# Performance work log

Measured on AMD Instinct MI355X. Metric: run time of the kernel, lower is better.

The kernel has to match this reference:

```python
import jax, jax.numpy as jnp
import numpy as np

E = 768   # embed_size
H = 64    # head_embed_size
B = 8
T = 4096  # == ctx_size


def setup_inputs() -> dict:
    key = jax.random.key(0)
    k1, k2, k3, k4 = jax.random.split(key, 4)
    inputs = jax.random.normal(k1, (B, T, E), dtype=jnp.float32)
    # Linear weights stored as (E, H) so projection is x @ W
    scale = 1.0 / np.sqrt(E)
    Wq = jax.random.uniform(k2, (E, H), dtype=jnp.float32, minval=-scale, maxval=scale)
    Wk = jax.random.uniform(k3, (E, H), dtype=jnp.float32, minval=-scale, maxval=scale)
    Wv = jax.random.uniform(k4, (E, H), dtype=jnp.float32, minval=-scale, maxval=scale)
    return {"inputs": inputs, "Wq": Wq, "Wk": Wk, "Wv": Wv}


def reference(inputs, Wq, Wk, Wv):
    Tlen = inputs.shape[1]
    q = inputs @ Wq  # (B,T,H)
    k = inputs @ Wk  # (B,T,H)
    v = inputs @ Wv  # (B,T,H)
    # NOTE: original module does NOT scale by 1/sqrt(H) — faithful reproduction.
    scores = jnp.einsum('bqh,bkh->bqk', q, k)  # (B,T,T)
    causal = jnp.tril(jnp.ones((Tlen, Tlen), dtype=bool))
    scores = jnp.where(causal, scores, -jnp.inf)
    attn = jax.nn.softmax(scores, axis=-1)
    # dropout=0 -> identity
    out = jnp.einsum('bqk,bkh->bqh', attn, v)  # (B,T,H)
    return out
```

## Files before the change

### kernel.cpp

```cpp
#include <hip/hip_runtime.h>
#include <hip/hip_bf16.h>

#define E_DIM 768
#define H_DIM 64
#define B_SZ 8
#define T_SZ 4096
#define BT (B_SZ * T_SZ)

typedef __attribute__((ext_vector_type(8))) short short8;
typedef __attribute__((ext_vector_type(4))) float floatx4;

#define RAWBAR() __asm__ volatile("s_waitcnt lgkmcnt(0)\n\ts_barrier" ::: "memory")

static __device__ __forceinline__ unsigned short bf1(float a) {
    __hip_bfloat16 h = __float2bfloat16(a);
    unsigned short u; __builtin_memcpy(&u, &h, 2); return u;
}
static __device__ __forceinline__ unsigned int pk2(float a, float b) {
    __hip_bfloat162 h = __float22bfloat162_rn(float2{a, b});
    unsigned int u; __builtin_memcpy(&u, &h, 4); return u;
}

__global__ __launch_bounds__(256) void prep_w(
    const float* __restrict__ Wq, const float* __restrict__ Wk,
    const float* __restrict__ Wv, unsigned short* __restrict__ Wt)
{
    __shared__ float Ls[64][65];
    const int nt = blockIdx.x;
    const int kc = blockIdx.y;
    const float* __restrict__ W = (nt == 0) ? Wq : (nt == 1) ? Wk : Wv;
    const float scl = (nt == 0) ? 1.44269504088896f : 1.0f;
    const int t = threadIdx.x;
    const int k0 = kc * 64;

#pragma unroll
    for (int it = 0; it < 16; ++it) {
        const int kk = (t >> 6) + it * 4;
        Ls[kk][t & 63] = W[(size_t)(k0 + kk) * H_DIM + (t & 63)];
    }
    __syncthreads();

#pragma unroll
    for (int it = 0; it < 4; ++it) {
        const int nl = (t >> 4) + it * 16;
        const int kl = (t & 15) * 4;
        unsigned int u[2];
        u[0] = pk2(Ls[kl + 0][nl] * scl, Ls[kl + 1][nl] * scl);
        u[1] = pk2(Ls[kl + 2][nl] * scl, Ls[kl + 3][nl] * scl);
        *(uint2*)(Wt + (size_t)(nt * 64 + nl) * E_DIM + k0 + kl) = *(uint2*)u;
    }
}

__global__ __launch_bounds__(768) void proj_mfma(
    const float* __restrict__ X, const unsigned short* __restrict__ Wt,
    unsigned short* __restrict__ Qb, unsigned short* __restrict__ Kb,
    unsigned short* __restrict__ Vtb)
{
    __shared__ unsigned short Xs[2][16][776];

    const int tid  = threadIdx.x;
    const int wave = tid >> 6, lane = tid & 63;
    const int row  = lane & 15, quad = lane >> 4;
    const int m0   = blockIdx.x * 128;

    short8 bfr[24];
    {
        const unsigned short* wp = Wt + (size_t)(wave * 16 + row) * E_DIM + quad * 8;
#pragma unroll
        for (int ks = 0; ks < 24; ++ks) bfr[ks] = *(const short8*)(wp + ks * 32);
    }

    const int srow = tid & 15;
    const int sc   = tid >> 4;
    const float* __restrict__ xbase = X + (size_t)(m0 + srow) * E_DIM + sc * 16;

    float4 fx[4];
#define LDX(mt)                                                               \
    {                                                                         \
        const float* p = xbase + (size_t)(mt) * 16 * E_DIM;                   \
        fx[0] = *(const float4*)(p);     fx[1] = *(const float4*)(p + 4);     \
        fx[2] = *(const float4*)(p + 8); fx[3] = *(const float4*)(p + 12);    \
    }
#define STX(buf)                                                              \
    {                                                                         \
        unsigned int tmp[8];                                                  \
        tmp[0] = pk2(fx[0].x, fx[0].y); tmp[1] = pk2(fx[0].z, fx[0].w);       \
        tmp[2] = pk2(fx[1].x, fx[1].y); tmp[3] = pk2(fx[1].z, fx[1].w);       \
        tmp[4] = pk2(fx[2].x, fx[2].y); tmp[5] = pk2(fx[2].z, fx[2].w);       \
        tmp[6] = pk2(fx[3].x, fx[3].y); tmp[7] = pk2(fx[3].z, fx[3].w);       \
        *(int4*)&Xs[buf][srow][sc * 16]     = *(int4*)&tmp[0];                \
        *(int4*)&Xs[buf][srow][sc * 16 + 8] = *(int4*)&tmp[4];                \
    }

    LDX(0); STX(0); LDX(1);
    RAWBAR();

    const int g  = wave >> 2;
    const int h  = (wave & 3) * 16 + row;
    unsigned short* __restrict__ OQK = (g == 0) ? Qb : Kb;
    const int bb = m0 >> 12;

    int cur = 0;
    for (int mt = 0; mt < 8; ++mt) {
        if (mt < 7) STX(cur ^ 1);
        if (mt < 6) LDX(mt + 2);

        floatx4 a0 = (floatx4)0.0f, a1 = (floatx4)0.0f;
        floatx4 a2 = (floatx4)0.0f, a3 = (floatx4)0.0f;
#pragma unroll
        for (int ks = 0; ks < 6; ++ks) {
            const short8 f0 = *(const short8*)&Xs[cur][row][(ks * 4 + 0) * 32 + quad * 8];
            const short8 f1 = *(const short8*)&Xs[cur][row][(ks * 4 + 1) * 32 + quad * 8];
            const short8 f2 = *(const short8*)&Xs[cur][row][(ks * 4 + 2) * 32 + quad * 8];
            const short8 f3 = *(const short8*)&Xs[cur][row][(ks * 4 + 3) * 32 + quad * 8];
            a0 = __builtin_amdgcn_mfma_f32_16x16x32_bf16(f0, bfr[ks * 4 + 0], a0, 0, 0, 0);
            a1 = __builtin_amdgcn_mfma_f32_16x16x32_bf16(f1, bfr[ks * 4 + 1], a1, 0, 0, 0);
            a2 = __builtin_amdgcn_mfma_f32_16x16x32_bf16(f2, bfr[ks * 4 + 2], a2, 0, 0, 0);
            a3 = __builtin_amdgcn_mfma_f32_16x16x32_bf16(f3, bfr[ks * 4 + 3], a3, 0, 0, 0);
        }
        floatx4 acc;
#pragma unroll
        for (int r = 0; r < 4; ++r) acc[r] = (a0[r] + a1[r]) + (a2[r] + a3[r]);

        const int mr = m0 + mt * 16 + quad * 4;
        if (g < 2) {
#pragma unroll
            for (int r = 0; r < 4; ++r)
                OQK[(size_t)(mr + r) * H_DIM + h] = bf1(acc[r]);
        } else {
            const int t0 = mr & 4095;
            unsigned int u[2];
            u[0] = pk2(acc[0], acc[1]); u[1] = pk2(acc[2], acc[3]);
            *(uint2*)(Vtb + ((size_t)bb * H_DIM + h) * T_SZ + t0) = *(uint2*)u;
        }

        RAWBAR();
        cur ^= 1;
    }
#undef LDX
#undef STX
}

__global__ __launch_bounds__(256, 6) void attn_mfma(
    const unsigned short* __restrict__ Qb,
    const unsigned short* __restrict__ Kb,
    const unsigned short* __restrict__ Vtb,
    float* __restrict__ Opart, float* __restrict__ lpart,
    float* __restrict__ Out)
{
    __shared__ __align__(16) unsigned short KV[2][64][72];

    const int lb = blockIdx.x;
    const int b  = lb & 7;
    const int s  = lb >> 3;
    int qq, c, m;
    if (s < 24)       { m = 6; qq = 60 + s / 6;                        c = s % 6; }
    else if (s < 84)  { m = 5; const int i = s - 24;  qq = 48 + i / 5;    c = i % 5; }
    else if (s < 132) { m = 4; const int i = s - 84;  qq = 36 + (i >> 2); c = i & 3; }
    else if (s < 168) { m = 3; const int i = s - 132; qq = 24 + i / 3;    c = i % 3; }
    else if (s < 192) { m = 2; const int i = s - 168; qq = 12 + (i >> 1); c = i & 1; }
    else              { m = 1; qq = s - 192; c = 0; }
    const int ntot = qq + 1;
    const int k0t  = (c * ntot) / m;
    const int k1t  = ((c + 1) * ntot) / m;
    const int ktd  = ntot - 1;
    const int n    = k1t - k0t;
    const bool split = (m > 1);

    const int tid  = threadIdx.x;
    const int wq   = tid >> 6;
    const int lane = tid & 63;
    const int col  = lane & 15, quad = lane >> 4;

    const size_t base = (size_t)b * T_SZ * H_DIM;
    const int q0  = qq * 64;

    short8 qf0, qf1;
    {
        const unsigned short* qp = Qb + base + (size_t)(q0 + wq * 16 + col) * H_DIM + quad * 8;
        qf0 = *(const short8*)(qp);
        qf1 = *(const short8*)(qp + 32);
    }

    floatx4 o[4];
#pragma unroll
    for (int i = 0; i < 4; ++i) o[i] = (floatx4)0.0f;
    float lp = 0.0f;

    const int krow = tid >> 2, kcol = (tid & 3) * 16;
    const int kprow = (krow & 32) + ((krow >> 2) & 1) * 16 + ((krow & 31) >> 3) * 4 + (krow & 3);
    const unsigned short* __restrict__ Ksrc = Kb + base + (size_t)krow * H_DIM + kcol;
    const unsigned short* __restrict__ Vsrc = Vtb + ((size_t)b * H_DIM + krow) * T_SZ + kcol;

    int4 kr0, kr1, vr0, vr1;
#define LDKV(t)                                                          \
    {                                                                    \
        const unsigned short* kp = Ksrc + (size_t)(t) * 64 * H_DIM;      \
        kr0 = *(const int4*)kp; kr1 = *(const int4*)(kp + 8);            \
        const unsigned short* vp = Vsrc + (t) * 64;                      \
        vr0 = *(const int4*)vp; vr1 = *(const int4*)(vp + 8);            \
    }
#define STKV()                                                           \
    {                                                                    \
        *(int4*)&KV[0][kprow][kcol] = kr0; *(int4*)&KV[0][kprow][kcol + 8] = kr1; \
        *(int4*)&KV[1][krow][kcol] = vr0; *(int4*)&KV[1][krow][kcol + 8] = vr1; \
    }

    LDKV(k0t);
    STKV();
    if (n > 1) LDKV(k0t + 1);
    RAWBAR();

    for (int i = 0; i < n; ++i) {
        const int kt = k0t + i;

#pragma unroll
        for (int j = 0; j < 2; ++j) {
            floatx4 a0 = (floatx4)0.0f, a1 = (floatx4)0.0f;
            __builtin_amdgcn_s_setprio(1);
            {
                const unsigned short* kp0 = &KV[0][j * 32 + col][quad * 8];
                const unsigned short* kp1 = &KV[0][j * 32 + 16 + col][quad * 8];
                a0 = __builtin_amdgcn_mfma_f32_16x16x32_bf16(*(const short8*)(kp0),      qf0, a0, 0, 0, 0);
                a1 = __builtin_amdgcn_mfma_f32_16x16x32_bf16(*(const short8*)(kp1),      qf0, a1, 0, 0, 0);
                a0 = __builtin_amdgcn_mfma_f32_16x16x32_bf16(*(const short8*)(kp0 + 32), qf1, a0, 0, 0, 0);
                a1 = __builtin_amdgcn_mfma_f32_16x16x32_bf16(*(const short8*)(kp1 + 32), qf1, a1, 0, 0, 0);
            }
            __builtin_amdgcn_s_setprio(0);

            if (kt == ktd) {
                const int qg = q0 + wq * 16 + col;
                const int kb = kt * 64 + j * 32 + quad * 8;
#pragma unroll
                for (int r = 0; r < 4; ++r) {
                    if (kb + r > qg)     a0[r] = -1e30f;
                    if (kb + 4 + r > qg) a1[r] = -1e30f;
                }
            }

            const float p0 = exp2f(a0[0]), p1 = exp2f(a0[1]), p2 = exp2f(a0[2]), p3 = exp2f(a0[3]);
            const float p4 = exp2f(a1[0]), p5 = exp2f(a1[1]), p6 = exp2f(a1[2]), p7 = exp2f(a1[3]);
            lp += ((p0 + p1) + (p2 + p3)) + ((p4 + p5) + (p6 + p7));
            unsigned int u0, u1, u2, u3;
            __asm__("v_cvt_pk_bf16_f32 %0, %1, %2" : "=v"(u0) : "v"(p0), "v"(p1));
            __asm__("v_cvt_pk_bf16_f32 %0, %1, %2" : "=v"(u1) : "v"(p2), "v"(p3));
            __asm__("v_cvt_pk_bf16_f32 %0, %1, %2" : "=v"(u2) : "v"(p4), "v"(p5));
            __asm__("v_cvt_pk_bf16_f32 %0, %1, %2" : "=v"(u3) : "v"(p6), "v"(p7));
            union { unsigned int u[4]; short8 v; } pu;
            pu.u[0] = u0; pu.u[1] = u1; pu.u[2] = u2; pu.u[3] = u3;
            const short8 pa = pu.v;

            __builtin_amdgcn_s_setprio(1);
#pragma unroll
            for (int d = 0; d < 4; ++d) {
                const short8 vb = *(const short8*)(&KV[1][d * 16 + col][j * 32 + quad * 8]);
                o[d] = __builtin_amdgcn_mfma_f32_16x16x32_bf16(pa, vb, o[d], 0, 0, 0);
            }
            __builtin_amdgcn_s_setprio(0);
        }

        RAWBAR();
        if (i + 1 < n) {
            STKV();
            if (i + 2 < n) LDKV(kt + 2);
        }
        RAWBAR();
    }

    lp += __shfl_xor(lp, 16);
    lp += __shfl_xor(lp, 32);
    float lr[4];
#pragma unroll
    for (int r = 0; r < 4; ++r) lr[r] = __shfl(lp, quad * 4 + r);

    if (!split) {
        float* op = Out + base + (size_t)(q0 + wq * 16 + quad * 4) * H_DIM;
#pragma unroll
        for (int r = 0; r < 4; ++r) {
            const float inv = 1.0f / lr[r];
#pragma unroll
            for (int d = 0; d < 4; ++d)
                op[(size_t)r * H_DIM + d * 16 + col] = o[d][r] * inv;
        }
    } else {
        const int pidx = (b * 64 + qq) * 6 + c;
        float* op = Opart + ((size_t)pidx * 64 + wq * 16 + quad * 4) * 64;
#pragma unroll
        for (int r = 0; r < 4; ++r)
#pragma unroll
            for (int d = 0; d < 4; ++d)
                op[(size_t)r * 64 + d * 16 + col] = o[d][r];
        if (quad == 0) lpart[pidx * 64 + wq * 16 + col] = lp;
    }
#undef LDKV
#undef STKV
}

__global__ __launch_bounds__(256) void attn_combine(
    const float* __restrict__ Opart, const float* __restrict__ lpart,
    float* __restrict__ Out)
{
    const int qq  = 12 + blockIdx.x;
    const int b   = blockIdx.y;
    const int m   = (qq + 12) / 12;
    const int tid = threadIdx.x;
    const int orow = tid >> 2;
    const int d0   = (tid & 3) * 16;
    const int p0   = (b * 64 + qq) * 6;

    float4 a0 = {0.f,0.f,0.f,0.f}, a1 = {0.f,0.f,0.f,0.f};
    float4 a2 = {0.f,0.f,0.f,0.f}, a3 = {0.f,0.f,0.f,0.f};
    float l = 0.0f;
    for (int j = 0; j < m; ++j) {
        const float* P = Opart + ((size_t)(p0 + j) * 64 + orow) * 64 + d0;
        const float4 b0 = *(const float4*)(P);
        const float4 b1 = *(const float4*)(P + 4);
        const float4 b2 = *(const float4*)(P + 8);
        const float4 b3 = *(const float4*)(P + 12);
        a0.x += b0.x; a0.y += b0.y; a0.z += b0.z; a0.w += b0.w;
        a1.x += b1.x; a1.y += b1.y; a1.z += b1.z; a1.w += b1.w;
        a2.x += b2.x; a2.y += b2.y; a2.z += b2.z; a2.w += b2.w;
        a3.x += b3.x; a3.y += b3.y; a3.z += b3.z; a3.w += b3.w;
        l += lpart[(p0 + j) * 64 + orow];
    }
    const float inv = 1.0f / l;
    a0.x *= inv; a0.y *= inv; a0.z *= inv; a0.w *= inv;
    a1.x *= inv; a1.y *= inv; a1.z *= inv; a1.w *= inv;
    a2.x *= inv; a2.y *= inv; a2.z *= inv; a2.w *= inv;
    a3.x *= inv; a3.y *= inv; a3.z *= inv; a3.w *= inv;

    float* op = Out + ((size_t)b * T_SZ + qq * 64 + orow) * H_DIM + d0;
    *(float4*)(op)      = a0;
    *(float4*)(op + 4)  = a1;
    *(float4*)(op + 8)  = a2;
    *(float4*)(op + 12) = a3;
}

extern "C" void kernel_launch(void* const* d_in, const int* in_sizes, int n_in,
                              void* d_out, int out_size, void* d_ws, size_t ws_size,
                              hipStream_t stream) {
    const float* X  = (const float*)d_in[0];
    const float* Wq = (const float*)d_in[1];
    const float* Wk = (const float*)d_in[2];
    const float* Wv = (const float*)d_in[3];

    unsigned short* Wt  = (unsigned short*)d_ws;
    unsigned short* Qb  = Wt + (size_t)192 * E_DIM;
    unsigned short* Kb  = Qb + (size_t)BT * H_DIM;
    unsigned short* Vtb = Kb + (size_t)BT * H_DIM;
    float* Opart = (float*)(Vtb + (size_t)BT * H_DIM);
    float* lpart = Opart + (size_t)3072 * 64 * 64;

    prep_w<<<dim3(3, 12), 256, 0, stream>>>(Wq, Wk, Wv, Wt);
    proj_mfma<<<256, 768, 0, stream>>>(X, Wt, Qb, Kb, Vtb);
    attn_mfma<<<1632, 256, 0, stream>>>(Qb, Kb, Vtb, Opart, lpart, (float*)d_out);
    attn_combine<<<dim3(52, 8), 256, 0, stream>>>(Opart, lpart, (float*)d_out);
}
```

Measured before the change: 213.8 us.

## Double query tile to 128 rows per block to reuse K/V tiles

```diff
diff --git a/kernel.cpp b/kernel.cpp
--- a/kernel.cpp
+++ b/kernel.cpp
@@ -141,7 +141,7 @@
 #undef STX
 }
 
-__global__ __launch_bounds__(256, 6) void attn_mfma(
+__global__ __launch_bounds__(256, 4) void attn_mfma(
     const unsigned short* __restrict__ Qb,
     const unsigned short* __restrict__ Kb,
     const unsigned short* __restrict__ Vtb,
@@ -154,16 +154,17 @@
     const int b  = lb & 7;
     const int s  = lb >> 3;
     int qq, c, m;
-    if (s < 24)       { m = 6; qq = 60 + s / 6;                        c = s % 6; }
-    else if (s < 84)  { m = 5; const int i = s - 24;  qq = 48 + i / 5;    c = i % 5; }
-    else if (s < 132) { m = 4; const int i = s - 84;  qq = 36 + (i >> 2); c = i & 3; }
-    else if (s < 168) { m = 3; const int i = s - 132; qq = 24 + i / 3;    c = i % 3; }
-    else if (s < 192) { m = 2; const int i = s - 168; qq = 12 + (i >> 1); c = i & 1; }
-    else              { m = 1; qq = s - 192; c = 0; }
-    const int ntot = qq + 1;
+    if (s < 32)       { m = 8; qq = 28 + (s >> 3);                   c = s & 7; }
+    else if (s < 60)  { m = 7; const int i = s - 32;  qq = 24 + i / 7;  c = i % 7; }
+    else if (s < 84)  { m = 6; const int i = s - 60;  qq = 20 + i / 6;  c = i % 6; }
+    else if (s < 104) { m = 5; const int i = s - 84;  qq = 16 + i / 5;  c = i % 5; }
+    else if (s < 120) { m = 4; const int i = s - 104; qq = 12 + (i >> 2); c = i & 3; }
+    else if (s < 132) { m = 3; const int i = s - 120; qq = 8 + i / 3;   c = i % 3; }
+    else if (s < 140) { m = 2; const int i = s - 132; qq = 4 + (i >> 1); c = i & 1; }
+    else              { m = 1; qq = s - 140; c = 0; }
+    const int ntot = 2 * (qq + 1);
     const int k0t  = (c * ntot) / m;
     const int k1t  = ((c + 1) * ntot) / m;
-    const int ktd  = ntot - 1;
     const int n    = k1t - k0t;
     const bool split = (m > 1);
 
@@ -173,19 +174,21 @@
     const int col  = lane & 15, quad = lane >> 4;
 
     const size_t base = (size_t)b * T_SZ * H_DIM;
-    const int q0  = qq * 64;
-
-    short8 qf0, qf1;
+    const int q0  = qq * 128;
+
+    short8 qfA0, qfA1, qfB0, qfB1;
     {
-        const unsigned short* qp = Qb + base + (size_t)(q0 + wq * 16 + col) * H_DIM + quad * 8;
-        qf0 = *(const short8*)(qp);
-        qf1 = *(const short8*)(qp + 32);
-    }
-
-    floatx4 o[4];
-#pragma unroll
-    for (int i = 0; i < 4; ++i) o[i] = (floatx4)0.0f;
-    float lp = 0.0f;
+        const unsigned short* qp = Qb + base + (size_t)(q0 + wq * 32 + col) * H_DIM + quad * 8;
+        qfA0 = *(const short8*)(qp);
+        qfA1 = *(const short8*)(qp + 32);
+        qfB0 = *(const short8*)(qp + 16 * H_DIM);
+        qfB1 = *(const short8*)(qp + 16 * H_DIM + 32);
+    }
+
+    floatx4 oA[4], oB[4];
+#pragma unroll
+    for (int i = 0; i < 4; ++i) { oA[i] = (floatx4)0.0f; oB[i] = (floatx4)0.0f; }
+    float lpA = 0.0f, lpB = 0.0f;
 
     const int krow = tid >> 2, kcol = (tid & 3) * 16;
     const int kprow = (krow & 32) + ((krow >> 2) & 1) * 16 + ((krow & 31) >> 3) * 4 + (krow & 3);
@@ -213,48 +216,73 @@
 
     for (int i = 0; i < n; ++i) {
         const int kt = k0t + i;
+        const bool dia = (kt >= ntot - 2);
 
 #pragma unroll
         for (int j = 0; j < 2; ++j) {
-            floatx4 a0 = (floatx4)0.0f, a1 = (floatx4)0.0f;
+            const unsigned short* kp0 = &KV[0][j * 32 + col][quad * 8];
+            const unsigned short* kp1 = &KV[0][j * 32 + 16 + col][quad * 8];
+            const short8 k0 = *(const short8*)(kp0);
+            const short8 k1 = *(const short8*)(kp0 + 32);
+            const short8 k2 = *(const short8*)(kp1);
+            const short8 k3 = *(const short8*)(kp1 + 32);
+
+            floatx4 aA0 = (floatx4)0.0f, aA1 = (floatx4)0.0f;
+            floatx4 aB0 = (floatx4)0.0f, aB1 = (floatx4)0.0f;
             __builtin_amdgcn_s_setprio(1);
-            {
-                const unsigned short* kp0 = &KV[0][j * 32 + col][quad * 8];
-                const unsigned short* kp1 = &KV[0][j * 32 + 16 + col][quad * 8];
-                a0 = __builtin_amdgcn_mfma_f32_16x16x32_bf16(*(const short8*)(kp0),      qf0, a0, 0, 0, 0);
-                a1 = __builtin_amdgcn_mfma_f32_16x16x32_bf16(*(const short8*)(kp1),      qf0, a1, 0, 0, 0);
-                a0 = __builtin_amdgcn_mfma_f32_16x16x32_bf16(*(const short8*)(kp0 + 32), qf1, a0, 0, 0, 0);
-                a1 = __builtin_amdgcn_mfma_f32_16x16x32_bf16(*(const short8*)(kp1 + 32), qf1, a1, 0, 0, 0);
-            }
+            aA0 = __builtin_amdgcn_mfma_f32_16x16x32_bf16(k0, qfA0, aA0, 0, 0, 0);
+            aA1 = __builtin_amdgcn_mfma_f32_16x16x32_bf16(k2, qfA0, aA1, 0, 0, 0);
+            aB0 = __builtin_amdgcn_mfma_f32_16x16x32_bf16(k0, qfB0, aB0, 0, 0, 0);
+            aB1 = __builtin_amdgcn_mfma_f32_16x16x32_bf16(k2, qfB0, aB1, 0, 0, 0);
+            aA0 = __builtin_amdgcn_mfma_f32_16x16x32_bf16(k1, qfA1, aA0, 0, 0, 0);
+            aA1 = __builtin_amdgcn_mfma_f32_16x16x32_bf16(k3, qfA1, aA1, 0, 0, 0);
+            aB0 = __builtin_amdgcn_mfma_f32_16x16x32_bf16(k1, qfB1, aB0, 0, 0, 0);
+            aB1 = __builtin_amdgcn_mfma_f32_16x16x32_bf16(k3, qfB1, aB1, 0, 0, 0);
             __builtin_amdgcn_s_setprio(0);
 
-            if (kt == ktd) {
-                const int qg = q0 + wq * 16 + col;
-                const int kb = kt * 64 + j * 32 + quad * 8;
+            if (dia) {
+                const int qgA = q0 + wq * 32 + col;
+                const int qgB = qgA + 16;
+                const int kb  = kt * 64 + j * 32 + quad * 8;
 #pragma unroll
                 for (int r = 0; r < 4; ++r) {
-                    if (kb + r > qg)     a0[r] = -1e30f;
-                    if (kb + 4 + r > qg) a1[r] = -1e30f;
+                    if (kb + r > qgA)     aA0[r] = -1e30f;
+                    if (kb + 4 + r > qgA) aA1[r] = -1e30f;
+                    if (kb + r > qgB)     aB0[r] = -1e30f;
+                    if (kb + 4 + r > qgB) aB1[r] = -1e30f;
                 }
             }
 
-            const float p0 = exp2f(a0[0]), p1 = exp2f(a0[1]), p2 = exp2f(a0[2]), p3 = exp2f(a0[3]);
-            const float p4 = exp2f(a1[0]), p5 = exp2f(a1[1]), p6 = exp2f(a1[2]), p7 = exp2f(a1[3]);
-            lp += ((p0 + p1) + (p2 + p3)) + ((p4 + p5) + (p6 + p7));
-            unsigned int u0, u1, u2, u3;
-            __asm__("v_cvt_pk_bf16_f32 %0, %1, %2" : "=v"(u0) : "v"(p0), "v"(p1));
-            __asm__("v_cvt_pk_bf16_f32 %0, %1, %2" : "=v"(u1) : "v"(p2), "v"(p3));
-            __asm__("v_cvt_pk_bf16_f32 %0, %1, %2" : "=v"(u2) : "v"(p4), "v"(p5));
-            __asm__("v_cvt_pk_bf16_f32 %0, %1, %2" : "=v"(u3) : "v"(p6), "v"(p7));
-            union { unsigned int u[4]; short8 v; } pu;
-            pu.u[0] = u0; pu.u[1] = u1; pu.u[2] = u2; pu.u[3] = u3;
-            const short8 pa = pu.v;
+            const float pA0 = exp2f(aA0[0]), pA1 = exp2f(aA0[1]), pA2 = exp2f(aA0[2]), pA3 = exp2f(aA0[3]);
+            const float pA4 = exp2f(aA1[0]), pA5 = exp2f(aA1[1]), pA6 = exp2f(aA1[2]), pA7 = exp2f(aA1[3]);
+            lpA += ((pA0 + pA1) + (pA2 + pA3)) + ((pA4 + pA5) + (pA6 + pA7));
+            unsigned int uA0, uA1, uA2, uA3;
+            __asm__("v_cvt_pk_bf16_f32 %0, %1, %2" : "=v"(uA0) : "v"(pA0), "v"(pA1));
+            __asm__("v_cvt_pk_bf16_f32 %0, %1, %2" : "=v"(uA1) : "v"(pA2), "v"(pA3));
+            __asm__("v_cvt_pk_bf16_f32 %0, %1, %2" : "=v"(uA2) : "v"(pA4), "v"(pA5));
+            __asm__("v_cvt_pk_bf16_f32 %0, %1, %2" : "=v"(uA3) : "v"(pA6), "v"(pA7));
+            union { unsigned int u[4]; short8 v; } puA;
+            puA.u[0] = uA0; puA.u[1] = uA1; puA.u[2] = uA2; puA.u[3] = uA3;
+            const short8 paA = puA.v;
+
+            const float pB0 = exp2f(aB0[0]), pB1 = exp2f(aB0[1]), pB2 = exp2f(aB0[2]), pB3 = exp2f(aB0[3]);
+            const float pB4 = exp2f(aB1[0]), pB5 = exp2f(aB1[1]), pB6 = exp2f(aB1[2]), pB7 = exp2f(aB1[3]);
+            lpB += ((pB0 + pB1) + (pB2 + pB3)) + ((pB4 + pB5) + (pB6 + pB7));
+            unsigned int uB0, uB1, uB2, uB3;
+            __asm__("v_cvt_pk_bf16_f32 %0, %1, %2" : "=v"(uB0) : "v"(pB0), "v"(pB1));
+            __asm__("v_cvt_pk_bf16_f32 %0, %1, %2" : "=v"(uB1) : "v"(pB2), "v"(pB3));
+            __asm__("v_cvt_pk_bf16_f32 %0, %1, %2" : "=v"(uB2) : "v"(pB4), "v"(pB5));
+            __asm__("v_cvt_pk_bf16_f32 %0, %1, %2" : "=v"(uB3) : "v"(pB6), "v"(pB7));
+            union { unsigned int u[4]; short8 v; } puB;
+            puB.u[0] = uB0; puB.u[1] = uB1; puB.u[2] = uB2; puB.u[3] = uB3;
+            const short8 paB = puB.v;
 
             __builtin_amdgcn_s_setprio(1);
 #pragma unroll
             for (int d = 0; d < 4; ++d) {
                 const short8 vb = *(const short8*)(&KV[1][d * 16 + col][j * 32 + quad * 8]);
-                o[d] = __builtin_amdgcn_mfma_f32_16x16x32_bf16(pa, vb, o[d], 0, 0, 0);
+                oA[d] = __builtin_amdgcn_mfma_f32_16x16x32_bf16(paA, vb, oA[d], 0, 0, 0);
+                oB[d] = __builtin_amdgcn_mfma_f32_16x16x32_bf16(paB, vb, oB[d], 0, 0, 0);
             }
             __builtin_amdgcn_s_setprio(0);
         }
@@ -267,30 +295,42 @@
         RAWBAR();
     }
 
-    lp += __shfl_xor(lp, 16);
-    lp += __shfl_xor(lp, 32);
-    float lr[4];
-#pragma unroll
-    for (int r = 0; r < 4; ++r) lr[r] = __shfl(lp, quad * 4 + r);
+    lpA += __shfl_xor(lpA, 16); lpA += __shfl_xor(lpA, 32);
+    lpB += __shfl_xor(lpB, 16); lpB += __shfl_xor(lpB, 32);
+    float lrA[4], lrB[4];
+#pragma unroll
+    for (int r = 0; r < 4; ++r) {
+        lrA[r] = __shfl(lpA, quad * 4 + r);
+        lrB[r] = __shfl(lpB, quad * 4 + r);
+    }
 
     if (!split) {
-        float* op = Out + base + (size_t)(q0 + wq * 16 + quad * 4) * H_DIM;
+        float* opA = Out + base + (size_t)(q0 + wq * 32 + quad * 4) * H_DIM;
+        float* opB = opA + (size_t)16 * H_DIM;
 #pragma unroll
         for (int r = 0; r < 4; ++r) {
-            const float inv = 1.0f / lr[r];
-#pragma unroll
-            for (int d = 0; d < 4; ++d)
-                op[(size_t)r * H_DIM + d * 16 + col] = o[d][r] * inv;
+            const float invA = 1.0f / lrA[r], invB = 1.0f / lrB[r];
+#pragma unroll
+            for (int d = 0; d < 4; ++d) {
+                opA[(size_t)r * H_DIM + d * 16 + col] = oA[d][r] * invA;
+                opB[(size_t)r * H_DIM + d * 16 + col] = oB[d][r] * invB;
+            }
         }
     } else {
-        const int pidx = (b * 64 + qq) * 6 + c;
-        float* op = Opart + ((size_t)pidx * 64 + wq * 16 + quad * 4) * 64;
+        const int pidx = (b * 32 + qq) * 8 + c;
+        float* opA = Opart + (size_t)pidx * 8192 + (wq * 32 + quad * 4) * 64;
+        float* opB = opA + 16 * 64;
 #pragma unroll
         for (int r = 0; r < 4; ++r)
 #pragma unroll
-            for (int d = 0; d < 4; ++d)
-                op[(size_t)r * 64 + d * 16 + col] = o[d][r];
-        if (quad == 0) lpart[pidx * 64 + wq * 16 + col] = lp;
+            for (int d = 0; d < 4; ++d) {
+                opA[(size_t)r * 64 + d * 16 + col] = oA[d][r];
+                opB[(size_t)r * 64 + d * 16 + col] = oB[d][r];
+            }
+        if (quad == 0) {
+            lpart[pidx * 128 + wq * 32 + col] = lpA;
+            lpart[pidx * 128 + wq * 32 + 16 + col] = lpB;
+        }
     }
 #undef LDKV
 #undef STKV
@@ -300,40 +340,34 @@
     const float* __restrict__ Opart, const float* __restrict__ lpart,
     float* __restrict__ Out)
 {
-    const int qq  = 12 + blockIdx.x;
+    const int qq  = 4 + blockIdx.x;
     const int b   = blockIdx.y;
-    const int m   = (qq + 12) / 12;
+    const int m   = (2 * qq + 9) / 8;
     const int tid = threadIdx.x;
-    const int orow = tid >> 2;
-    const int d0   = (tid & 3) * 16;
-    const int p0   = (b * 64 + qq) * 6;
-
-    float4 a0 = {0.f,0.f,0.f,0.f}, a1 = {0.f,0.f,0.f,0.f};
-    float4 a2 = {0.f,0.f,0.f,0.f}, a3 = {0.f,0.f,0.f,0.f};
+    const int orow = tid >> 1;
+    const int d0   = (tid & 1) * 32;
+    const int p0   = (b * 32 + qq) * 8;
+
+    float4 a[8];
+#pragma unroll
+    for (int i = 0; i < 8; ++i) a[i] = float4{0.f, 0.f, 0.f, 0.f};
     float l = 0.0f;
     for (int j = 0; j < m; ++j) {
-        const float* P = Opart + ((size_t)(p0 + j) * 64 + orow) * 64 + d0;
-        const float4 b0 = *(const float4*)(P);
-        const float4 b1 = *(const float4*)(P + 4);
-        const float4 b2 = *(const float4*)(P + 8);
-        const float4 b3 = *(const float4*)(P + 12);
-        a0.x += b0.x; a0.y += b0.y; a0.z += b0.z; a0.w += b0.w;
-        a1.x += b1.x; a1.y += b1.y; a1.z += b1.z; a1.w += b1.w;
-        a2.x += b2.x; a2.y += b2.y; a2.z += b2.z; a2.w += b2.w;
-        a3.x += b3.x; a3.y += b3.y; a3.z += b3.z; a3.w += b3.w;
-        l += lpart[(p0 + j) * 64 + orow];
+        const float* P = Opart + (size_t)(p0 + j) * 8192 + orow * 64 + d0;
+#pragma unroll
+        for (int i = 0; i < 8; ++i) {
+            const float4 v = *(const float4*)(P + i * 4);
+            a[i].x += v.x; a[i].y += v.y; a[i].z += v.z; a[i].w += v.w;
+        }
+        l += lpart[(p0 + j) * 128 + orow];
     }
     const float inv = 1.0f / l;
-    a0.x *= inv; a0.y *= inv; a0.z *= inv; a0.w *= inv;
-    a1.x *= inv; a1.y *= inv; a1.z *= inv; a1.w *= inv;
-    a2.x *= inv; a2.y *= inv; a2.z *= inv; a2.w *= inv;
-    a3.x *= inv; a3.y *= inv; a3.z *= inv; a3.w *= inv;
-
-    float* op = Out + ((size_t)b * T_SZ + qq * 64 + orow) * H_DIM + d0;
-    *(float4*)(op)      = a0;
-    *(float4*)(op + 4)  = a1;
-    *(float4*)(op + 8)  = a2;
-    *(float4*)(op + 12) = a3;
+    float* op = Out + ((size_t)b * T_SZ + qq * 128 + orow) * H_DIM + d0;
+#pragma unroll
+    for (int i = 0; i < 8; ++i) {
+        a[i].x *= inv; a[i].y *= inv; a[i].z *= inv; a[i].w *= inv;
+        *(float4*)(op + i * 4) = a[i];
+    }
 }
 
 extern "C" void kernel_launch(void* const* d_in, const int* in_sizes, int n_in,
@@ -349,10 +383,10 @@
     unsigned short* Kb  = Qb + (size_t)BT * H_DIM;
     unsigned short* Vtb = Kb + (size_t)BT * H_DIM;
     float* Opart = (float*)(Vtb + (size_t)BT * H_DIM);
-    float* lpart = Opart + (size_t)3072 * 64 * 64;
+    float* lpart = Opart + (size_t)2048 * 8192;
 
     prep_w<<<dim3(3, 12), 256, 0, stream>>>(Wq, Wk, Wv, Wt);
     proj_mfma<<<256, 768, 0, stream>>>(X, Wt, Qb, Kb, Vtb);
-    attn_mfma<<<1632, 256, 0, stream>>>(Qb, Kb, Vtb, Opart, lpart, (float*)d_out);
-    attn_combine<<<dim3(52, 8), 256, 0, stream>>>(Opart, lpart, (float*)d_out);
-}
+    attn_mfma<<<1152, 256, 0, stream>>>(Qb, Kb, Vtb, Opart, lpart, (float*)d_out);
+    attn_combine<<<dim3(28, 8), 256, 0, stream>>>(Opart, lpart, (float*)d_out);
+}
```

Measured after the change: 215.9 us. No clear change (+1.0%).
